# Kernel tuning notes

Measured on AMD Instinct MI355X. Metric: run time of the kernel, lower is better.

The kernel has to match this reference:

```python
import jax, jax.numpy as jnp
import numpy as np
import math

EMSIZE = 1024
B, S = 4, 1024
N = B * S

def setup_inputs() -> dict:
    key = jax.random.key(0)
    k1, k2, k3, k4, k5 = jax.random.split(key, 5)
    x = jax.random.normal(k1, (B, S, EMSIZE), dtype=jnp.float32)
    mask = jax.random.randint(k2, (N, N), 0, 2, dtype=jnp.int32)
    # nn.Linear default init scale ~ 1/sqrt(fan_in); use small normal weights
    sc = 1.0 / math.sqrt(EMSIZE)
    Wq = jax.random.normal(k3, (EMSIZE, EMSIZE), dtype=jnp.float32) * sc
    Wk = jax.random.normal(k4, (EMSIZE, EMSIZE), dtype=jnp.float32) * sc
    Wv = jax.random.normal(k5, (EMSIZE, EMSIZE), dtype=jnp.float32) * sc
    return {"x": x, "mask": mask, "Wq": Wq, "Wk": Wk, "Wv": Wv}

def reference(x, mask, Wq, Wk, Wv):
    b, s, e = x.shape
    xf = x.reshape(b * s, e)                       # [N, E]
    q = xf @ Wq.T                                  # nn.Linear: x @ W^T
    k = xf @ Wk.T
    v = xf @ Wv.T
    sim = q @ k.T                                  # [N, N] full cross-batch scores
    sim = jnp.where(mask == 0, jnp.float32(-1e20), sim)
    # NOTE: original scales AFTER masking, matching masked_fill then divide
    attn = jax.nn.softmax(sim / math.sqrt(e), axis=-1)
    out = attn @ v                                 # [N, E]
    return out.reshape(b, s, e)
```

## Files before the change

### kernel.cpp

```cpp
#include <hip/hip_runtime.h>
#include <hip/hip_bf16.h>
#include <math.h>


typedef __attribute__((ext_vector_type(8))) __bf16 bf16x8;
typedef __attribute__((ext_vector_type(4))) __bf16 bf16x4;
typedef __attribute__((ext_vector_type(4))) float f32x4;

__device__ __forceinline__ void gload_lds16(const void* g, void* l) {
  __builtin_amdgcn_global_load_lds(
      (__attribute__((address_space(1))) void*)(g),
      (__attribute__((address_space(3))) void*)(l), 16, 0, 0);
}

#define WAITB(N) asm volatile("s_waitcnt vmcnt(" #N ")\ns_barrier" ::: "memory")


#define STQ_A(buf, j, kt)                                                   \
  { int p = tid + (j) * 512; int row = p >> 2; int cg = (p & 3) ^ (row & 3);\
    gload_lds16(A + (row0 + row) * lda + (kt) * 32 + cg * 8,                \
                sA + (buf) * 8192 + p * 8); }
#define STQ_B(buf, j, kt)                                                   \
  { int p = tid + (j) * 512; int row = p >> 2; int cg = (p & 3) ^ (row & 3);\
    gload_lds16(B + (col0 + row) * ldb + (kt) * 32 + cg * 8,                \
                sB + (buf) * 8192 + p * 8); }

#define LDS_FRAG(base, r) \
  *(const bf16x8*)((base) + (r) * 32 + (((hi) ^ ((r) & 3)) * 8))

#define MM16(mq, AF)                                                        \
  __builtin_amdgcn_s_setprio(1);                                            \
  _Pragma("unroll") for (int m = 0; m < 4; ++m)                             \
    _Pragma("unroll") for (int n = 0; n < 4; ++n)                           \
      acc[(mq) * 4 + m][n] = __builtin_amdgcn_mfma_f32_16x16x32_bf16(       \
          AF[m], bfr[n], acc[(mq) * 4 + m][n], 0, 0, 0);                    \
  __builtin_amdgcn_s_setprio(0);

__device__ __forceinline__ void g8_loop(const __bf16* __restrict__ A, long lda, long row0,
                                        const __bf16* __restrict__ B, long ldb, long col0,
                                        int kt0, __bf16* sA, __bf16* sB,
                                        f32x4 (&acc)[8][4], int tid) {
  const int lane = tid & 63;
  const int w = tid >> 6;
  const int wr = w >> 2, wc = w & 3;
  const int lo = lane & 15, hi = lane >> 4;
  const int NT = 32;

#pragma unroll
  for (int t = 0; t < 3; ++t) {
    STQ_A(t, 0, kt0 + t); STQ_A(t, 1, kt0 + t);
    STQ_B(t, 0, kt0 + t); STQ_B(t, 1, kt0 + t);
  }
  WAITB(8);

  for (int t = 0; t < NT; ++t) {
    const int d = t & 3;
    const __bf16* sAc = sA + d * 8192;
    const __bf16* sBc = sB + d * 8192;
    const int s = (t + 3) & 3;
    bf16x8 af[4], af2[4], bfr[4];
#pragma unroll
    for (int m = 0; m < 4; ++m) af[m] = LDS_FRAG(sAc, wr * 128 + m * 16 + lo);
#pragma unroll
    for (int n = 0; n < 4; ++n) bfr[n] = LDS_FRAG(sBc, wc * 64 + n * 16 + lo);
    if (t + 3 < NT) { STQ_A(s, 0, kt0 + t + 3); STQ_A(s, 1, kt0 + t + 3); }
    __builtin_amdgcn_s_barrier();
    MM16(0, af);
    __builtin_amdgcn_s_barrier();
#pragma unroll
    for (int m = 0; m < 4; ++m) af2[m] = LDS_FRAG(sAc, wr * 128 + 64 + m * 16 + lo);
    if (t + 3 < NT) { STQ_B(s, 0, kt0 + t + 3); STQ_B(s, 1, kt0 + t + 3); }
    __builtin_amdgcn_s_barrier();
    MM16(1, af2);
    if (t + 3 < NT)      { WAITB(8); }
    else if (t + 2 < NT) { WAITB(4); }
    else                 { WAITB(0); }
  }
}


__global__ __launch_bounds__(512) void qkv8(const __bf16* __restrict__ xb,
                                            const __bf16* __restrict__ wq,
                                            const __bf16* __restrict__ wk,
                                            const __bf16* __restrict__ wv,
                                            __bf16* __restrict__ qb,
                                            __bf16* __restrict__ kb,
                                            __bf16* __restrict__ vtb) {
  __shared__ __bf16 sA[4 * 8192];
  __shared__ __bf16 sB[4 * 8192];
  const int raw = blockIdx.x;
  const int wid = (raw & 7) * 24 + (raw >> 3);
  const int z = wid >> 6;
  const int r2 = wid & 63;
  const int tid = threadIdx.x;
  const __bf16* A;
  const __bf16* B;
  long row0, col0;
  if (z == 2) {
    A = wv; B = xb;
    row0 = (long)(r2 >> 4) * 256;
    col0 = (long)(r2 & 15) * 256;
  } else {
    A = xb; B = (z == 0) ? wq : wk;
    row0 = (long)(r2 >> 2) * 256;
    col0 = (long)(r2 & 3) * 256;
  }
  const long lda = 1024, ldb = 1024;
  f32x4 acc[8][4] = {};
  g8_loop(A, lda, row0, B, ldb, col0, 0, sA, sB, acc, tid);

  const int lane = tid & 63, w = tid >> 6;
  const int wr = w >> 2, wc = w & 3;
  const int lo = lane & 15, hi = lane >> 4;
#pragma unroll
  for (int m = 0; m < 8; ++m)
#pragma unroll
    for (int n = 0; n < 4; ++n)
#pragma unroll
      for (int i = 0; i < 4; ++i) {
        long r = row0 + wr * 128 + m * 16 + hi * 4 + i;
        long c = col0 + wc * 64 + n * 16 + lo;
        __bf16 v = (__bf16)acc[m][n][i];
        if (z == 0)      qb[r * 1024 + c] = v;
        else if (z == 1) kb[r * 1024 + c] = v;
        else             vtb[r * 4096 + c] = v;
      }
}

__global__ __launch_bounds__(512) void qk8(const __bf16* __restrict__ qb,
                                           const __bf16* __restrict__ kb,
                                           __bf16* __restrict__ sim) {
  __shared__ __bf16 sA[4 * 8192];
  __shared__ __bf16 sB[4 * 8192];
  const int raw = blockIdx.x;
  const int wid = (raw & 7) * 32 + (raw >> 3);
  const long row0 = (long)(wid >> 4) * 256;
  const long col0 = (long)(wid & 15) * 256;
  const int tid = threadIdx.x;
  const __bf16* A = qb;
  const __bf16* B = kb;
  const long lda = 1024, ldb = 1024;
  f32x4 acc[8][4] = {};
  g8_loop(A, lda, row0, B, ldb, col0, 0, sA, sB, acc, tid);

  const int lane = tid & 63, w = tid >> 6;
  const int wr = w >> 2, wc = w & 3;
  const int lo = lane & 15, hi = lane >> 4;
#pragma unroll
  for (int m = 0; m < 8; ++m)
#pragma unroll
    for (int n = 0; n < 4; ++n)
#pragma unroll
      for (int i = 0; i < 4; ++i) {
        long r = row0 + wr * 128 + m * 16 + hi * 4 + i;
        long c = col0 + wc * 64 + n * 16 + lo;
        sim[r * 4096 + c] = (__bf16)acc[m][n][i];
      }
}

__global__ __launch_bounds__(512) void pv8(const __bf16* __restrict__ attn,
                                           const __bf16* __restrict__ vt,
                                           float* __restrict__ out,
                                           float* __restrict__ p1,
                                           float* __restrict__ p2,
                                           float* __restrict__ p3) {
  __shared__ __bf16 sA[4 * 8192];
  __shared__ __bf16 sB[4 * 8192];
  const int raw = blockIdx.x;
  const int wid = (raw & 7) * 32 + (raw >> 3);
  const int z = wid >> 6;
  const int r2 = wid & 63;
  const long row0 = (long)(r2 >> 2) * 256;
  const long col0 = (long)(r2 & 3) * 256;
  float* C = (z == 0) ? out : (z == 1) ? p1 : (z == 2) ? p2 : p3;
  const int tid = threadIdx.x;
  const __bf16* A = attn;
  const __bf16* B = vt;
  const long lda = 4096, ldb = 4096;
  f32x4 acc[8][4] = {};
  g8_loop(A, lda, row0, B, ldb, col0, z * 32, sA, sB, acc, tid);

  const int lane = tid & 63, w = tid >> 6;
  const int wr = w >> 2, wc = w & 3;
  const int lo = lane & 15, hi = lane >> 4;
#pragma unroll
  for (int m = 0; m < 8; ++m)
#pragma unroll
    for (int n = 0; n < 4; ++n)
#pragma unroll
      for (int i = 0; i < 4; ++i) {
        long r = row0 + wr * 128 + m * 16 + hi * 4 + i;
        long c = col0 + wc * 64 + n * 16 + lo;
        C[r * 1024 + c] = acc[m][n][i];
      }
}

__global__ __launch_bounds__(256) void reduce_add4(float* __restrict__ out,
                                                   const float* __restrict__ a,
                                                   const float* __restrict__ b,
                                                   const float* __restrict__ c) {
  int i = blockIdx.x * 256 + threadIdx.x;
  float4 o = ((const float4*)out)[i];
  float4 x = ((const float4*)a)[i];
  float4 y = ((const float4*)b)[i];
  float4 z = ((const float4*)c)[i];
  o.x += x.x + y.x + z.x; o.y += x.y + y.y + z.y;
  o.z += x.z + y.z + z.z; o.w += x.w + y.w + z.w;
  ((float4*)out)[i] = o;
}

__global__ __launch_bounds__(256) void cvt_all(const float* __restrict__ x,
                                               const float* __restrict__ wq,
                                               const float* __restrict__ wk,
                                               const float* __restrict__ wv,
                                               __bf16* __restrict__ xb,
                                               __bf16* __restrict__ wqb,
                                               __bf16* __restrict__ wkb,
                                               __bf16* __restrict__ wvb) {
  int b = blockIdx.x;
  const float* in;
  __bf16* out;
  int base;
  if (b < 4096)      { in = x;  out = xb;  base = b; }
  else if (b < 5120) { in = wq; out = wqb; base = b - 4096; }
  else if (b < 6144) { in = wk; out = wkb; base = b - 5120; }
  else               { in = wv; out = wvb; base = b - 6144; }
  int i = base * 256 + threadIdx.x;
  float4 f = ((const float4*)in)[i];
  bf16x4 o;
  o[0] = (__bf16)f.x; o[1] = (__bf16)f.y; o[2] = (__bf16)f.z; o[3] = (__bf16)f.w;
  ((bf16x4*)out)[i] = o;
}

__global__ __launch_bounds__(256) void softmax_rows(__bf16* __restrict__ sim,
                                                    const int* __restrict__ mask) {
  const int row = blockIdx.x;
  __bf16* rp = sim + (size_t)row * 4096;
  const int4* mrow = (const int4*)(mask + (size_t)row * 4096);
  const int tid = threadIdx.x;

  float vals[16];
  float lmax = -INFINITY;
#pragma unroll
  for (int j = 0; j < 2; ++j) {
    bf16x8 s = ((const bf16x8*)rp)[tid + 256 * j];
    int4 m0 = mrow[(tid + 256 * j) * 2];
    int4 m1 = mrow[(tid + 256 * j) * 2 + 1];
    float f[8];
#pragma unroll
    for (int e = 0; e < 8; ++e) f[e] = (float)s[e];
    f[0] = m0.x ? f[0] : -1e20f;  f[1] = m0.y ? f[1] : -1e20f;
    f[2] = m0.z ? f[2] : -1e20f;  f[3] = m0.w ? f[3] : -1e20f;
    f[4] = m1.x ? f[4] : -1e20f;  f[5] = m1.y ? f[5] : -1e20f;
    f[6] = m1.z ? f[6] : -1e20f;  f[7] = m1.w ? f[7] : -1e20f;
#pragma unroll
    for (int e = 0; e < 8; ++e) {
      vals[8 * j + e] = f[e];
      lmax = fmaxf(lmax, f[e]);
    }
  }
#pragma unroll
  for (int off = 32; off; off >>= 1) lmax = fmaxf(lmax, __shfl_xor(lmax, off));
  __shared__ float red[4];
  __shared__ float bro[2];
  if ((tid & 63) == 0) red[tid >> 6] = lmax;
  __syncthreads();
  if (tid == 0) bro[0] = fmaxf(fmaxf(red[0], red[1]), fmaxf(red[2], red[3]));
  __syncthreads();
  const float m = bro[0];

  float e[16];
  float lsum = 0.f;
#pragma unroll
  for (int j = 0; j < 16; ++j) {
    e[j] = __expf((vals[j] - m) * 0.03125f);
    lsum += e[j];
  }
#pragma unroll
  for (int off = 32; off; off >>= 1) lsum += __shfl_xor(lsum, off);
  if ((tid & 63) == 0) red[tid >> 6] = lsum;
  __syncthreads();
  if (tid == 0) bro[1] = red[0] + red[1] + red[2] + red[3];
  __syncthreads();
  const float inv = 1.0f / bro[1];

#pragma unroll
  for (int j = 0; j < 2; ++j) {
    bf16x8 o;
#pragma unroll
    for (int q = 0; q < 8; ++q) o[q] = (__bf16)(e[8 * j + q] * inv);
    ((bf16x8*)rp)[tid + 256 * j] = o;
  }
}

extern "C" void kernel_launch(void* const* d_in, const int* in_sizes, int n_in,
                              void* d_out, int out_size, void* d_ws, size_t ws_size,
                              hipStream_t stream) {
  const float* x = (const float*)d_in[0];
  const int* mask = (const int*)d_in[1];
  const float* Wq = (const float*)d_in[2];
  const float* Wk = (const float*)d_in[3];
  const float* Wv = (const float*)d_in[4];
  float* out = (float*)d_out;

  char* ws = (char*)d_ws;
  __bf16* vtb = (__bf16*)(ws);
  __bf16* xb  = (__bf16*)(ws + (8ull << 20));
  __bf16* wqb = (__bf16*)(ws + (16ull << 20));
  __bf16* wkb = (__bf16*)(ws + (18ull << 20));
  __bf16* wvb = (__bf16*)(ws + (20ull << 20));
  __bf16* qb  = (__bf16*)(ws + (22ull << 20));
  __bf16* kb  = (__bf16*)(ws + (30ull << 20));
  __bf16* sim = (__bf16*)(ws + (38ull << 20));
  float*  p1  = (float*)(ws + (8ull << 20));
  float*  p2  = (float*)(ws + (70ull << 20));
  float*  p3  = (float*)(ws + (86ull << 20));

  cvt_all<<<7168, 256, 0, stream>>>(x, Wq, Wk, Wv, xb, wqb, wkb, wvb);

  dim3 blk(512);
  qkv8<<<192, blk, 0, stream>>>(xb, wqb, wkb, wvb, qb, kb, vtb);
  qk8<<<256, blk, 0, stream>>>(qb, kb, sim);
  softmax_rows<<<4096, 256, 0, stream>>>(sim, mask);
  pv8<<<256, blk, 0, stream>>>(sim, vtb, out, p1, p2, p3);
  reduce_add4<<<4096, 256, 0, stream>>>(out, p1, p2, p3);
}
```

Measured before the change: 162.6 us.

## Fuse masked softmax into QK epilogue without max subtraction, defer normalization

The separate softmax pass is removed. The QK GEMM epilogue now applies the mask, exponentiates the scaled scores directly without subtracting a row max, writes unnormalized bf16 probabilities, and accumulates row sums through atomics. The PV GEMM switches to 128-row tiles with a 2-way split-K instead of 4-way, and the final reduce divides by the row sum. This cuts a full read-modify-write pass over the 4096x4096 score matrix and halves the partial buffers. It risks overflow when scores are large, since the max is no longer subtracted, and adds atomic traffic.

Measured after the change: 157.7 us. 3.1% less time.

```diff
diff --git a/kernel.cpp b/kernel.cpp
--- a/kernel.cpp
+++ b/kernel.cpp
@@ -14,16 +14,6 @@
 }
 
 #define WAITB(N) asm volatile("s_waitcnt vmcnt(" #N ")\ns_barrier" ::: "memory")
-
-
-#define STQ_A(buf, j, kt)                                                   \
-  { int p = tid + (j) * 512; int row = p >> 2; int cg = (p & 3) ^ (row & 3);\
-    gload_lds16(A + (row0 + row) * lda + (kt) * 32 + cg * 8,                \
-                sA + (buf) * 8192 + p * 8); }
-#define STQ_B(buf, j, kt)                                                   \
-  { int p = tid + (j) * 512; int row = p >> 2; int cg = (p & 3) ^ (row & 3);\
-    gload_lds16(B + (col0 + row) * ldb + (kt) * 32 + cg * 8,                \
-                sB + (buf) * 8192 + p * 8); }
 
 #define LDS_FRAG(base, r) \
   *(const bf16x8*)((base) + (r) * 32 + (((hi) ^ ((r) & 3)) * 8))
@@ -36,44 +26,66 @@
           AF[m], bfr[n], acc[(mq) * 4 + m][n], 0, 0, 0);                    \
   __builtin_amdgcn_s_setprio(0);
 
+template <int MR, int NT>
 __device__ __forceinline__ void g8_loop(const __bf16* __restrict__ A, long lda, long row0,
                                         const __bf16* __restrict__ B, long ldb, long col0,
                                         int kt0, __bf16* sA, __bf16* sB,
-                                        f32x4 (&acc)[8][4], int tid) {
+                                        f32x4 (&acc)[MR][4], int tid) {
   const int lane = tid & 63;
   const int w = tid >> 6;
   const int wr = w >> 2, wc = w & 3;
   const int lo = lane & 15, hi = lane >> 4;
-  const int NT = 32;
-
-#pragma unroll
-  for (int t = 0; t < 3; ++t) {
-    STQ_A(t, 0, kt0 + t); STQ_A(t, 1, kt0 + t);
-    STQ_B(t, 0, kt0 + t); STQ_B(t, 1, kt0 + t);
-  }
-  WAITB(8);
+  constexpr int ATILE = MR * 1024;
+  constexpr int AL = MR / 4;
+
+  auto stageA = [&](int buf, int kt) {
+#pragma unroll
+    for (int j = 0; j < AL; ++j) {
+      int p = tid + j * 512;
+      int row = p >> 2, cg = (p & 3) ^ (row & 3);
+      gload_lds16(A + (row0 + row) * lda + kt * 32 + cg * 8,
+                  sA + buf * ATILE + p * 8);
+    }
+  };
+  auto stageB = [&](int buf, int kt) {
+#pragma unroll
+    for (int j = 0; j < 2; ++j) {
+      int p = tid + j * 512;
+      int row = p >> 2, cg = (p & 3) ^ (row & 3);
+      gload_lds16(B + (col0 + row) * ldb + kt * 32 + cg * 8,
+                  sB + buf * 8192 + p * 8);
+    }
+  };
+
+#pragma unroll
+  for (int t = 0; t < 3; ++t) { stageA(t, kt0 + t); stageB(t, kt0 + t); }
+  if constexpr (MR == 8) { WAITB(8); } else { WAITB(6); }
 
   for (int t = 0; t < NT; ++t) {
     const int d = t & 3;
-    const __bf16* sAc = sA + d * 8192;
+    const __bf16* sAc = sA + d * ATILE;
     const __bf16* sBc = sB + d * 8192;
     const int s = (t + 3) & 3;
-    bf16x8 af[4], af2[4], bfr[4];
-#pragma unroll
-    for (int m = 0; m < 4; ++m) af[m] = LDS_FRAG(sAc, wr * 128 + m * 16 + lo);
+    bf16x8 af[4], bfr[4];
+#pragma unroll
+    for (int m = 0; m < 4; ++m) af[m] = LDS_FRAG(sAc, wr * (MR * 16) + m * 16 + lo);
 #pragma unroll
     for (int n = 0; n < 4; ++n) bfr[n] = LDS_FRAG(sBc, wc * 64 + n * 16 + lo);
-    if (t + 3 < NT) { STQ_A(s, 0, kt0 + t + 3); STQ_A(s, 1, kt0 + t + 3); }
+    if (t + 3 < NT) stageA(s, kt0 + t + 3);
+    if (MR == 4 && t + 3 < NT) stageB(s, kt0 + t + 3);
     __builtin_amdgcn_s_barrier();
     MM16(0, af);
-    __builtin_amdgcn_s_barrier();
-#pragma unroll
-    for (int m = 0; m < 4; ++m) af2[m] = LDS_FRAG(sAc, wr * 128 + 64 + m * 16 + lo);
-    if (t + 3 < NT) { STQ_B(s, 0, kt0 + t + 3); STQ_B(s, 1, kt0 + t + 3); }
-    __builtin_amdgcn_s_barrier();
-    MM16(1, af2);
-    if (t + 3 < NT)      { WAITB(8); }
-    else if (t + 2 < NT) { WAITB(4); }
+    if constexpr (MR == 8) {
+      __builtin_amdgcn_s_barrier();
+      bf16x8 af2[4];
+#pragma unroll
+      for (int m = 0; m < 4; ++m) af2[m] = LDS_FRAG(sAc, wr * 128 + 64 + m * 16 + lo);
+      if (t + 3 < NT) stageB(s, kt0 + t + 3);
+      __builtin_amdgcn_s_barrier();
+      MM16(1, af2);
+    }
+    if (t + 3 < NT)      { if constexpr (MR == 8) { WAITB(8); } else { WAITB(6); } }
+    else if (t + 2 < NT) { if constexpr (MR == 8) { WAITB(4); } else { WAITB(3); } }
     else                 { WAITB(0); }
   }
 }
@@ -105,9 +117,8 @@
     row0 = (long)(r2 >> 2) * 256;
     col0 = (long)(r2 & 3) * 256;
   }
-  const long lda = 1024, ldb = 1024;
   f32x4 acc[8][4] = {};
-  g8_loop(A, lda, row0, B, ldb, col0, 0, sA, sB, acc, tid);
+  g8_loop<8, 32>(A, 1024, row0, B, 1024, col0, 0, sA, sB, acc, tid);
 
   const int lane = tid & 63, w = tid >> 6;
   const int wr = w >> 2, wc = w & 3;
@@ -129,7 +140,9 @@
 
 __global__ __launch_bounds__(512) void qk8(const __bf16* __restrict__ qb,
                                            const __bf16* __restrict__ kb,
-                                           __bf16* __restrict__ sim) {
+                                           const int* __restrict__ mask,
+                                           __bf16* __restrict__ attn,
+                                           float* __restrict__ rowsum) {
   __shared__ __bf16 sA[4 * 8192];
   __shared__ __bf16 sB[4 * 8192];
   const int raw = blockIdx.x;
@@ -137,11 +150,8 @@
   const long row0 = (long)(wid >> 4) * 256;
   const long col0 = (long)(wid & 15) * 256;
   const int tid = threadIdx.x;
-  const __bf16* A = qb;
-  const __bf16* B = kb;
-  const long lda = 1024, ldb = 1024;
   f32x4 acc[8][4] = {};
-  g8_loop(A, lda, row0, B, ldb, col0, 0, sA, sB, acc, tid);
+  g8_loop<8, 32>(qb, 1024, row0, kb, 1024, col0, 0, sA, sB, acc, tid);
 
   const int lane = tid & 63, w = tid >> 6;
   const int wr = w >> 2, wc = w & 3;
@@ -149,64 +159,66 @@
 #pragma unroll
   for (int m = 0; m < 8; ++m)
 #pragma unroll
-    for (int n = 0; n < 4; ++n)
-#pragma unroll
-      for (int i = 0; i < 4; ++i) {
-        long r = row0 + wr * 128 + m * 16 + hi * 4 + i;
+    for (int i = 0; i < 4; ++i) {
+      long r = row0 + wr * 128 + m * 16 + hi * 4 + i;
+      float s = 0.f;
+#pragma unroll
+      for (int n = 0; n < 4; ++n) {
         long c = col0 + wc * 64 + n * 16 + lo;
-        sim[r * 4096 + c] = (__bf16)acc[m][n][i];
+        int mk = mask[r * 4096 + c];
+        float p = mk ? __expf(acc[m][n][i] * 0.03125f) : 0.f;
+        attn[r * 4096 + c] = (__bf16)p;
+        s += p;
       }
+      s += __shfl_xor(s, 1); s += __shfl_xor(s, 2);
+      s += __shfl_xor(s, 4); s += __shfl_xor(s, 8);
+      if (lo == 0) atomicAdd(&rowsum[r], s);
+    }
 }
 
 __global__ __launch_bounds__(512) void pv8(const __bf16* __restrict__ attn,
                                            const __bf16* __restrict__ vt,
                                            float* __restrict__ out,
-                                           float* __restrict__ p1,
-                                           float* __restrict__ p2,
-                                           float* __restrict__ p3) {
-  __shared__ __bf16 sA[4 * 8192];
+                                           float* __restrict__ p1) {
+  __shared__ __bf16 sA[4 * 4096];
   __shared__ __bf16 sB[4 * 8192];
   const int raw = blockIdx.x;
   const int wid = (raw & 7) * 32 + (raw >> 3);
-  const int z = wid >> 6;
-  const int r2 = wid & 63;
-  const long row0 = (long)(r2 >> 2) * 256;
+  const int z = wid >> 7;
+  const int r2 = wid & 127;
+  const long row0 = (long)(r2 >> 2) * 128;
   const long col0 = (long)(r2 & 3) * 256;
-  float* C = (z == 0) ? out : (z == 1) ? p1 : (z == 2) ? p2 : p3;
+  float* C = z ? p1 : out;
   const int tid = threadIdx.x;
-  const __bf16* A = attn;
-  const __bf16* B = vt;
-  const long lda = 4096, ldb = 4096;
-  f32x4 acc[8][4] = {};
-  g8_loop(A, lda, row0, B, ldb, col0, z * 32, sA, sB, acc, tid);
+  f32x4 acc[4][4] = {};
+  g8_loop<4, 64>(attn, 4096, row0, vt, 4096, col0, z * 64, sA, sB, acc, tid);
 
   const int lane = tid & 63, w = tid >> 6;
   const int wr = w >> 2, wc = w & 3;
   const int lo = lane & 15, hi = lane >> 4;
 #pragma unroll
-  for (int m = 0; m < 8; ++m)
+  for (int m = 0; m < 4; ++m)
 #pragma unroll
     for (int n = 0; n < 4; ++n)
 #pragma unroll
       for (int i = 0; i < 4; ++i) {
-        long r = row0 + wr * 128 + m * 16 + hi * 4 + i;
+        long r = row0 + wr * 64 + m * 16 + hi * 4 + i;
         long c = col0 + wc * 64 + n * 16 + lo;
         C[r * 1024 + c] = acc[m][n][i];
       }
 }
 
-__global__ __launch_bounds__(256) void reduce_add4(float* __restrict__ out,
-                                                   const float* __restrict__ a,
-                                                   const float* __restrict__ b,
-                                                   const float* __restrict__ c) {
+__global__ __launch_bounds__(256) void reduce_add2(float* __restrict__ out,
+                                                   const float* __restrict__ p1,
+                                                   const float* __restrict__ rs) {
   int i = blockIdx.x * 256 + threadIdx.x;
-  float4 o = ((const float4*)out)[i];
-  float4 x = ((const float4*)a)[i];
-  float4 y = ((const float4*)b)[i];
-  float4 z = ((const float4*)c)[i];
-  o.x += x.x + y.x + z.x; o.y += x.y + y.y + z.y;
-  o.z += x.z + y.z + z.z; o.w += x.w + y.w + z.w;
-  ((float4*)out)[i] = o;
+  int row = i >> 8;
+  float inv = 1.0f / rs[row];
+  float4 a = ((const float4*)out)[i];
+  float4 b = ((const float4*)p1)[i];
+  a.x = (a.x + b.x) * inv; a.y = (a.y + b.y) * inv;
+  a.z = (a.z + b.z) * inv; a.w = (a.w + b.w) * inv;
+  ((float4*)out)[i] = a;
 }
 
 __global__ __launch_bounds__(256) void cvt_all(const float* __restrict__ x,
@@ -216,8 +228,14 @@
                                                __bf16* __restrict__ xb,
                                                __bf16* __restrict__ wqb,
                                                __bf16* __restrict__ wkb,
-                                               __bf16* __restrict__ wvb) {
+                                               __bf16* __restrict__ wvb,
+                                               float* __restrict__ rowsum) {
   int b = blockIdx.x;
+  if (b >= 7168) {
+#pragma unroll
+    for (int j = 0; j < 16; ++j) rowsum[threadIdx.x * 16 + j] = 0.f;
+    return;
+  }
   const float* in;
   __bf16* out;
   int base;
@@ -232,67 +250,6 @@
   ((bf16x4*)out)[i] = o;
 }
 
-__global__ __launch_bounds__(256) void softmax_rows(__bf16* __restrict__ sim,
-                                                    const int* __restrict__ mask) {
-  const int row = blockIdx.x;
-  __bf16* rp = sim + (size_t)row * 4096;
-  const int4* mrow = (const int4*)(mask + (size_t)row * 4096);
-  const int tid = threadIdx.x;
-
-  float vals[16];
-  float lmax = -INFINITY;
-#pragma unroll
-  for (int j = 0; j < 2; ++j) {
-    bf16x8 s = ((const bf16x8*)rp)[tid + 256 * j];
-    int4 m0 = mrow[(tid + 256 * j) * 2];
-    int4 m1 = mrow[(tid + 256 * j) * 2 + 1];
-    float f[8];
-#pragma unroll
-    for (int e = 0; e < 8; ++e) f[e] = (float)s[e];
-    f[0] = m0.x ? f[0] : -1e20f;  f[1] = m0.y ? f[1] : -1e20f;
-    f[2] = m0.z ? f[2] : -1e20f;  f[3] = m0.w ? f[3] : -1e20f;
-    f[4] = m1.x ? f[4] : -1e20f;  f[5] = m1.y ? f[5] : -1e20f;
-    f[6] = m1.z ? f[6] : -1e20f;  f[7] = m1.w ? f[7] : -1e20f;
-#pragma unroll
-    for (int e = 0; e < 8; ++e) {
-      vals[8 * j + e] = f[e];
-      lmax = fmaxf(lmax, f[e]);
-    }
-  }
-#pragma unroll
-  for (int off = 32; off; off >>= 1) lmax = fmaxf(lmax, __shfl_xor(lmax, off));
-  __shared__ float red[4];
-  __shared__ float bro[2];
-  if ((tid & 63) == 0) red[tid >> 6] = lmax;
-  __syncthreads();
-  if (tid == 0) bro[0] = fmaxf(fmaxf(red[0], red[1]), fmaxf(red[2], red[3]));
-  __syncthreads();
-  const float m = bro[0];
-
-  float e[16];
-  float lsum = 0.f;
-#pragma unroll
-  for (int j = 0; j < 16; ++j) {
-    e[j] = __expf((vals[j] - m) * 0.03125f);
-    lsum += e[j];
-  }
-#pragma unroll
-  for (int off = 32; off; off >>= 1) lsum += __shfl_xor(lsum, off);
-  if ((tid & 63) == 0) red[tid >> 6] = lsum;
-  __syncthreads();
-  if (tid == 0) bro[1] = red[0] + red[1] + red[2] + red[3];
-  __syncthreads();
-  const float inv = 1.0f / bro[1];
-
-#pragma unroll
-  for (int j = 0; j < 2; ++j) {
-    bf16x8 o;
-#pragma unroll
-    for (int q = 0; q < 8; ++q) o[q] = (__bf16)(e[8 * j + q] * inv);
-    ((bf16x8*)rp)[tid + 256 * j] = o;
-  }
-}
-
 extern "C" void kernel_launch(void* const* d_in, const int* in_sizes, int n_in,
                               void* d_out, int out_size, void* d_ws, size_t ws_size,
                               hipStream_t stream) {
@@ -311,17 +268,15 @@
   __bf16* wvb = (__bf16*)(ws + (20ull << 20));
   __bf16* qb  = (__bf16*)(ws + (22ull << 20));
   __bf16* kb  = (__bf16*)(ws + (30ull << 20));
-  __bf16* sim = (__bf16*)(ws + (38ull << 20));
+  __bf16* attn = (__bf16*)(ws + (38ull << 20));
+  float*  rowsum = (float*)(ws + (70ull << 20));
   float*  p1  = (float*)(ws + (8ull << 20));
-  float*  p2  = (float*)(ws + (70ull << 20));
-  float*  p3  = (float*)(ws + (86ull << 20));
-
-  cvt_all<<<7168, 256, 0, stream>>>(x, Wq, Wk, Wv, xb, wqb, wkb, wvb);
+
+  cvt_all<<<7169, 256, 0, stream>>>(x, Wq, Wk, Wv, xb, wqb, wkb, wvb, rowsum);
 
   dim3 blk(512);
   qkv8<<<192, blk, 0, stream>>>(xb, wqb, wkb, wvb, qb, kb, vtb);
-  qk8<<<256, blk, 0, stream>>>(qb, kb, sim);
-  softmax_rows<<<4096, 256, 0, stream>>>(sim, mask);
-  pv8<<<256, blk, 0, stream>>>(sim, vtb, out, p1, p2, p3);
-  reduce_add4<<<4096, 256, 0, stream>>>(out, p1, p2, p3);
-}
+  qk8<<<256, blk, 0, stream>>>(qb, kb, mask, attn, rowsum);
+  pv8<<<256, blk, 0, stream>>>(attn, vtb, out, p1);
+  reduce_add2<<<4096, 256, 0, stream>>>(out, p1, rowsum);
+}
```

## Replace split-K PV GEMM with 128x128 full-K tiles, drop reduction pass

Applied to the files above, without the earlier changes.

The PV GEMM no longer splits K four ways into partial fp32 buffers followed by a reduce_add4 kernel. A new pv4 kernel uses 128x128 tiles with 256 threads and loops over the full K=4096, writing the output directly. The aim is to remove the partial-sum traffic and the extra launch. The change also alters the LDS swizzle to XOR with (row>>1)&3 and remaps qk8 blocks to XCD-local 2D tiles for better L2 reuse. In exchange, each PV block runs a much longer serial K loop with a smaller tile, which lowers arithmetic intensity per block.

Measured after the change: 155.4 us. 1.05x faster.

```diff
diff --git a/kernel.cpp b/kernel.cpp
--- a/kernel.cpp
+++ b/kernel.cpp
@@ -15,18 +15,8 @@
 
 #define WAITB(N) asm volatile("s_waitcnt vmcnt(" #N ")\ns_barrier" ::: "memory")
 
-
-#define STQ_A(buf, j, kt)                                                   \
-  { int p = tid + (j) * 512; int row = p >> 2; int cg = (p & 3) ^ (row & 3);\
-    gload_lds16(A + (row0 + row) * lda + (kt) * 32 + cg * 8,                \
-                sA + (buf) * 8192 + p * 8); }
-#define STQ_B(buf, j, kt)                                                   \
-  { int p = tid + (j) * 512; int row = p >> 2; int cg = (p & 3) ^ (row & 3);\
-    gload_lds16(B + (col0 + row) * ldb + (kt) * 32 + cg * 8,                \
-                sB + (buf) * 8192 + p * 8); }
-
 #define LDS_FRAG(base, r) \
-  *(const bf16x8*)((base) + (r) * 32 + (((hi) ^ ((r) & 3)) * 8))
+  *(const bf16x8*)((base) + (r) * 32 + (((hi) ^ (((r) >> 1) & 3)) * 8))
 
 #define MM16(mq, AF)                                                        \
   __builtin_amdgcn_s_setprio(1);                                            \
@@ -36,6 +26,7 @@
           AF[m], bfr[n], acc[(mq) * 4 + m][n], 0, 0, 0);                    \
   __builtin_amdgcn_s_setprio(0);
 
+template <int NT>
 __device__ __forceinline__ void g8_loop(const __bf16* __restrict__ A, long lda, long row0,
                                         const __bf16* __restrict__ B, long ldb, long col0,
                                         int kt0, __bf16* sA, __bf16* sB,
@@ -44,13 +35,28 @@
   const int w = tid >> 6;
   const int wr = w >> 2, wc = w & 3;
   const int lo = lane & 15, hi = lane >> 4;
-  const int NT = 32;
-
-#pragma unroll
-  for (int t = 0; t < 3; ++t) {
-    STQ_A(t, 0, kt0 + t); STQ_A(t, 1, kt0 + t);
-    STQ_B(t, 0, kt0 + t); STQ_B(t, 1, kt0 + t);
-  }
+
+  auto stageA = [&](int buf, int kt) {
+#pragma unroll
+    for (int j = 0; j < 2; ++j) {
+      int p = tid + j * 512;
+      int row = p >> 2, cg = (p & 3) ^ ((row >> 1) & 3);
+      gload_lds16(A + (row0 + row) * lda + kt * 32 + cg * 8,
+                  sA + buf * 8192 + p * 8);
+    }
+  };
+  auto stageB = [&](int buf, int kt) {
+#pragma unroll
+    for (int j = 0; j < 2; ++j) {
+      int p = tid + j * 512;
+      int row = p >> 2, cg = (p & 3) ^ ((row >> 1) & 3);
+      gload_lds16(B + (col0 + row) * ldb + kt * 32 + cg * 8,
+                  sB + buf * 8192 + p * 8);
+    }
+  };
+
+#pragma unroll
+  for (int t = 0; t < 3; ++t) { stageA(t, kt0 + t); stageB(t, kt0 + t); }
   WAITB(8);
 
   for (int t = 0; t < NT; ++t) {
@@ -58,18 +64,19 @@
     const __bf16* sAc = sA + d * 8192;
     const __bf16* sBc = sB + d * 8192;
     const int s = (t + 3) & 3;
-    bf16x8 af[4], af2[4], bfr[4];
+    bf16x8 af[4], bfr[4];
 #pragma unroll
     for (int m = 0; m < 4; ++m) af[m] = LDS_FRAG(sAc, wr * 128 + m * 16 + lo);
 #pragma unroll
     for (int n = 0; n < 4; ++n) bfr[n] = LDS_FRAG(sBc, wc * 64 + n * 16 + lo);
-    if (t + 3 < NT) { STQ_A(s, 0, kt0 + t + 3); STQ_A(s, 1, kt0 + t + 3); }
+    if (t + 3 < NT) stageA(s, kt0 + t + 3);
     __builtin_amdgcn_s_barrier();
     MM16(0, af);
     __builtin_amdgcn_s_barrier();
+    bf16x8 af2[4];
 #pragma unroll
     for (int m = 0; m < 4; ++m) af2[m] = LDS_FRAG(sAc, wr * 128 + 64 + m * 16 + lo);
-    if (t + 3 < NT) { STQ_B(s, 0, kt0 + t + 3); STQ_B(s, 1, kt0 + t + 3); }
+    if (t + 3 < NT) stageB(s, kt0 + t + 3);
     __builtin_amdgcn_s_barrier();
     MM16(1, af2);
     if (t + 3 < NT)      { WAITB(8); }
@@ -105,9 +112,8 @@
     row0 = (long)(r2 >> 2) * 256;
     col0 = (long)(r2 & 3) * 256;
   }
-  const long lda = 1024, ldb = 1024;
   f32x4 acc[8][4] = {};
-  g8_loop(A, lda, row0, B, ldb, col0, 0, sA, sB, acc, tid);
+  g8_loop<32>(A, 1024, row0, B, 1024, col0, 0, sA, sB, acc, tid);
 
   const int lane = tid & 63, w = tid >> 6;
   const int wr = w >> 2, wc = w & 3;
@@ -133,15 +139,14 @@
   __shared__ __bf16 sA[4 * 8192];
   __shared__ __bf16 sB[4 * 8192];
   const int raw = blockIdx.x;
-  const int wid = (raw & 7) * 32 + (raw >> 3);
-  const long row0 = (long)(wid >> 4) * 256;
-  const long col0 = (long)(wid & 15) * 256;
+  const int xcd = raw & 7, idx = raw >> 3;
+  const int rp = (xcd >> 1) * 4 + (idx >> 3);
+  const int cp = (xcd & 1) * 8 + (idx & 7);
+  const long row0 = (long)rp * 256;
+  const long col0 = (long)cp * 256;
   const int tid = threadIdx.x;
-  const __bf16* A = qb;
-  const __bf16* B = kb;
-  const long lda = 1024, ldb = 1024;
   f32x4 acc[8][4] = {};
-  g8_loop(A, lda, row0, B, ldb, col0, 0, sA, sB, acc, tid);
+  g8_loop<32>(qb, 1024, row0, kb, 1024, col0, 0, sA, sB, acc, tid);
 
   const int lane = tid & 63, w = tid >> 6;
   const int wr = w >> 2, wc = w & 3;
@@ -158,55 +163,143 @@
       }
 }
 
-__global__ __launch_bounds__(512) void pv8(const __bf16* __restrict__ attn,
+__global__ __launch_bounds__(256) void pv4(const __bf16* __restrict__ attn,
                                            const __bf16* __restrict__ vt,
-                                           float* __restrict__ out,
-                                           float* __restrict__ p1,
-                                           float* __restrict__ p2,
-                                           float* __restrict__ p3) {
-  __shared__ __bf16 sA[4 * 8192];
-  __shared__ __bf16 sB[4 * 8192];
+                                           float* __restrict__ out) {
+  __shared__ __bf16 sA[4 * 4096];
+  __shared__ __bf16 sB[4 * 4096];
   const int raw = blockIdx.x;
-  const int wid = (raw & 7) * 32 + (raw >> 3);
-  const int z = wid >> 6;
-  const int r2 = wid & 63;
-  const long row0 = (long)(r2 >> 2) * 256;
-  const long col0 = (long)(r2 & 3) * 256;
-  float* C = (z == 0) ? out : (z == 1) ? p1 : (z == 2) ? p2 : p3;
+  const int xcd = raw & 7, idx = raw >> 3;
+  const int rp = (xcd >> 1) * 8 + (idx >> 2);
+  const int cp = (xcd & 1) * 4 + (idx & 3);
+  const long row0 = (long)rp * 128;
+  const long col0 = (long)cp * 128;
   const int tid = threadIdx.x;
-  const __bf16* A = attn;
-  const __bf16* B = vt;
-  const long lda = 4096, ldb = 4096;
-  f32x4 acc[8][4] = {};
-  g8_loop(A, lda, row0, B, ldb, col0, z * 32, sA, sB, acc, tid);
-
   const int lane = tid & 63, w = tid >> 6;
-  const int wr = w >> 2, wc = w & 3;
+  const int wr = w >> 1, wc = w & 1;
   const int lo = lane & 15, hi = lane >> 4;
-#pragma unroll
-  for (int m = 0; m < 8; ++m)
+  constexpr int NT = 128;
+
+  auto stageA = [&](int buf, int kt) {
+#pragma unroll
+    for (int j = 0; j < 2; ++j) {
+      int p = tid + j * 256;
+      int row = p >> 2, cg = (p & 3) ^ ((row >> 1) & 3);
+      gload_lds16(attn + (row0 + row) * 4096 + kt * 32 + cg * 8,
+                  sA + buf * 4096 + p * 8);
+    }
+  };
+  auto stageB = [&](int buf, int kt) {
+#pragma unroll
+    for (int j = 0; j < 2; ++j) {
+      int p = tid + j * 256;
+      int row = p >> 2, cg = (p & 3) ^ ((row >> 1) & 3);
+      gload_lds16(vt + (col0 + row) * 4096 + kt * 32 + cg * 8,
+                  sB + buf * 4096 + p * 8);
+    }
+  };
+
+  f32x4 acc[4][4] = {};
+#pragma unroll
+  for (int t = 0; t < 3; ++t) { stageA(t, t); stageB(t, t); }
+  WAITB(8);
+
+#pragma unroll 4
+  for (int t = 0; t < NT; ++t) {
+    const int d = t & 3;
+    const __bf16* sAc = sA + d * 4096;
+    const __bf16* sBc = sB + d * 4096;
+    const int s = (t + 3) & 3;
+    bf16x8 af[4], bfr[4];
+#pragma unroll
+    for (int m = 0; m < 4; ++m) af[m] = LDS_FRAG(sAc, wr * 64 + m * 16 + lo);
+#pragma unroll
+    for (int n = 0; n < 4; ++n) bfr[n] = LDS_FRAG(sBc, wc * 64 + n * 16 + lo);
+    if (t + 3 < NT) { stageA(s, t + 3); stageB(s, t + 3); }
+    __builtin_amdgcn_s_barrier();
+    __builtin_amdgcn_s_setprio(1);
+#pragma unroll
+    for (int m = 0; m < 4; ++m)
+#pragma unroll
+      for (int n = 0; n < 4; ++n)
+        acc[m][n] = __builtin_amdgcn_mfma_f32_16x16x32_bf16(af[m], bfr[n], acc[m][n], 0, 0, 0);
+    __builtin_amdgcn_s_setprio(0);
+    if (t + 3 < NT)      { WAITB(8); }
+    else if (t + 2 < NT) { WAITB(4); }
+    else                 { WAITB(0); }
+  }
+
+#pragma unroll
+  for (int m = 0; m < 4; ++m)
 #pragma unroll
     for (int n = 0; n < 4; ++n)
 #pragma unroll
       for (int i = 0; i < 4; ++i) {
-        long r = row0 + wr * 128 + m * 16 + hi * 4 + i;
+        long r = row0 + wr * 64 + m * 16 + hi * 4 + i;
         long c = col0 + wc * 64 + n * 16 + lo;
-        C[r * 1024 + c] = acc[m][n][i];
+        out[r * 1024 + c] = acc[m][n][i];
       }
 }
 
-__global__ __launch_bounds__(256) void reduce_add4(float* __restrict__ out,
-                                                   const float* __restrict__ a,
-                                                   const float* __restrict__ b,
-                                                   const float* __restrict__ c) {
-  int i = blockIdx.x * 256 + threadIdx.x;
-  float4 o = ((const float4*)out)[i];
-  float4 x = ((const float4*)a)[i];
-  float4 y = ((const float4*)b)[i];
-  float4 z = ((const float4*)c)[i];
-  o.x += x.x + y.x + z.x; o.y += x.y + y.y + z.y;
-  o.z += x.z + y.z + z.z; o.w += x.w + y.w + z.w;
-  ((float4*)out)[i] = o;
+__global__ __launch_bounds__(256) void softmax_rows(__bf16* __restrict__ sim,
+                                                    const int* __restrict__ mask) {
+  const int row = blockIdx.x;
+  __bf16* rp = sim + (size_t)row * 4096;
+  const int4* mrow = (const int4*)(mask + (size_t)row * 4096);
+  const int tid = threadIdx.x;
+
+  float vals[16];
+  float lmax = -INFINITY;
+#pragma unroll
+  for (int j = 0; j < 2; ++j) {
+    bf16x8 s = ((const bf16x8*)rp)[tid + 256 * j];
+    int4 m0 = mrow[(tid + 256 * j) * 2];
+    int4 m1 = mrow[(tid + 256 * j) * 2 + 1];
+    float f[8];
+#pragma unroll
+    for (int e = 0; e < 8; ++e) f[e] = (float)s[e];
+    f[0] = m0.x ? f[0] : -1e20f;  f[1] = m0.y ? f[1] : -1e20f;
+    f[2] = m0.z ? f[2] : -1e20f;  f[3] = m0.w ? f[3] : -1e20f;
+    f[4] = m1.x ? f[4] : -1e20f;  f[5] = m1.y ? f[5] : -1e20f;
+    f[6] = m1.z ? f[6] : -1e20f;  f[7] = m1.w ? f[7] : -1e20f;
+#pragma unroll
+    for (int e = 0; e < 8; ++e) {
+      vals[8 * j + e] = f[e];
+      lmax = fmaxf(lmax, f[e]);
+    }
+  }
+#pragma unroll
+  for (int off = 32; off; off >>= 1) lmax = fmaxf(lmax, __shfl_xor(lmax, off));
+  __shared__ float red[4];
+  __shared__ float bro[2];
+  if ((tid & 63) == 0) red[tid >> 6] = lmax;
+  __syncthreads();
+  if (tid == 0) bro[0] = fmaxf(fmaxf(red[0], red[1]), fmaxf(red[2], red[3]));
+  __syncthreads();
+  const float m = bro[0];
+
+  float e[16];
+  float lsum = 0.f;
+#pragma unroll
+  for (int j = 0; j < 16; ++j) {
+    e[j] = __expf((vals[j] - m) * 0.03125f);
+    lsum += e[j];
+  }
+#pragma unroll
+  for (int off = 32; off; off >>= 1) lsum += __shfl_xor(lsum, off);
+  if ((tid & 63) == 0) red[tid >> 6] = lsum;
+  __syncthreads();
+  if (tid == 0) bro[1] = red[0] + red[1] + red[2] + red[3];
+  __syncthreads();
+  const float inv = 1.0f / bro[1];
+
+#pragma unroll
+  for (int j = 0; j < 2; ++j) {
+    bf16x8 o;
+#pragma unroll
+    for (int q = 0; q < 8; ++q) o[q] = (__bf16)(e[8 * j + q] * inv);
+    ((bf16x8*)rp)[tid + 256 * j] = o;
+  }
 }
 
 __global__ __launch_bounds__(256) void cvt_all(const float* __restrict__ x,
@@ -232,67 +325,6 @@
   ((bf16x4*)out)[i] = o;
 }
 
-__global__ __launch_bounds__(256) void softmax_rows(__bf16* __restrict__ sim,
-                                                    const int* __restrict__ mask) {
-  const int row = blockIdx.x;
-  __bf16* rp = sim + (size_t)row * 4096;
-  const int4* mrow = (const int4*)(mask + (size_t)row * 4096);
-  const int tid = threadIdx.x;
-
-  float vals[16];
-  float lmax = -INFINITY;
-#pragma unroll
-  for (int j = 0; j < 2; ++j) {
-    bf16x8 s = ((const bf16x8*)rp)[tid + 256 * j];
-    int4 m0 = mrow[(tid + 256 * j) * 2];
-    int4 m1 = mrow[(tid + 256 * j) * 2 + 1];
-    float f[8];
-#pragma unroll
-    for (int e = 0; e < 8; ++e) f[e] = (float)s[e];
-    f[0] = m0.x ? f[0] : -1e20f;  f[1] = m0.y ? f[1] : -1e20f;
-    f[2] = m0.z ? f[2] : -1e20f;  f[3] = m0.w ? f[3] : -1e20f;
-    f[4] = m1.x ? f[4] : -1e20f;  f[5] = m1.y ? f[5] : -1e20f;
-    f[6] = m1.z ? f[6] : -1e20f;  f[7] = m1.w ? f[7] : -1e20f;
-#pragma unroll
-    for (int e = 0; e < 8; ++e) {
-      vals[8 * j + e] = f[e];
-      lmax = fmaxf(lmax, f[e]);
-    }
-  }
-#pragma unroll
-  for (int off = 32; off; off >>= 1) lmax = fmaxf(lmax, __shfl_xor(lmax, off));
-  __shared__ float red[4];
-  __shared__ float bro[2];
-  if ((tid & 63) == 0) red[tid >> 6] = lmax;
-  __syncthreads();
-  if (tid == 0) bro[0] = fmaxf(fmaxf(red[0], red[1]), fmaxf(red[2], red[3]));
-  __syncthreads();
-  const float m = bro[0];
-
-  float e[16];
-  float lsum = 0.f;
-#pragma unroll
-  for (int j = 0; j < 16; ++j) {
-    e[j] = __expf((vals[j] - m) * 0.03125f);
-    lsum += e[j];
-  }
-#pragma unroll
-  for (int off = 32; off; off >>= 1) lsum += __shfl_xor(lsum, off);
-  if ((tid & 63) == 0) red[tid >> 6] = lsum;
-  __syncthreads();
-  if (tid == 0) bro[1] = red[0] + red[1] + red[2] + red[3];
-  __syncthreads();
-  const float inv = 1.0f / bro[1];
-
-#pragma unroll
-  for (int j = 0; j < 2; ++j) {
-    bf16x8 o;
-#pragma unroll
-    for (int q = 0; q < 8; ++q) o[q] = (__bf16)(e[8 * j + q] * inv);
-    ((bf16x8*)rp)[tid + 256 * j] = o;
-  }
-}
-
 extern "C" void kernel_launch(void* const* d_in, const int* in_sizes, int n_in,
                               void* d_out, int out_size, void* d_ws, size_t ws_size,
                               hipStream_t stream) {
@@ -312,16 +344,11 @@
   __bf16* qb  = (__bf16*)(ws + (22ull << 20));
   __bf16* kb  = (__bf16*)(ws + (30ull << 20));
   __bf16* sim = (__bf16*)(ws + (38ull << 20));
-  float*  p1  = (float*)(ws + (8ull << 20));
-  float*  p2  = (float*)(ws + (70ull << 20));
-  float*  p3  = (float*)(ws + (86ull << 20));
 
   cvt_all<<<7168, 256, 0, stream>>>(x, Wq, Wk, Wv, xb, wqb, wkb, wvb);
 
-  dim3 blk(512);
-  qkv8<<<192, blk, 0, stream>>>(xb, wqb, wkb, wvb, qb, kb, vtb);
-  qk8<<<256, blk, 0, stream>>>(qb, kb, sim);
+  qkv8<<<192, 512, 0, stream>>>(xb, wqb, wkb, wvb, qb, kb, vtb);
+  qk8<<<256, 512, 0, stream>>>(qb, kb, sim);
   softmax_rows<<<4096, 256, 0, stream>>>(sim, mask);
-  pv8<<<256, blk, 0, stream>>>(sim, vtb, out, p1, p2, p3);
-  reduce_add4<<<4096, 256, 0, stream>>>(out, p1, p2, p3);
-}
+  pv4<<<256, 256, 0, stream>>>(sim, vtb, out);
+}
```
